# Kernel tuning notes

Measured on AMD Instinct MI355X. Metric: run time of the kernel, lower is better.

The kernel has to match this reference:

```python
import jax, jax.numpy as jnp
import numpy as np

N = 40000      # nodes
E = 640000     # edges
IN_C = 128
HID = 256
OUT_C = 10
G = 64         # graphs in batch


def setup_inputs() -> dict:
    key = jax.random.key(0)
    ks = jax.random.split(key, 8)
    x = jax.random.normal(ks[0], (N, IN_C), dtype=jnp.float32)
    edge_index = jax.random.randint(ks[1], (2, E), 0, N, dtype=jnp.int64)
    batch = jnp.sort(jax.random.randint(ks[2], (N,), 0, G, dtype=jnp.int64))
    W1 = jax.random.normal(ks[3], (IN_C, HID), dtype=jnp.float32) / np.sqrt(IN_C)
    b1 = jnp.zeros((HID,), dtype=jnp.float32)
    W2 = jax.random.normal(ks[4], (HID, HID), dtype=jnp.float32) / np.sqrt(HID)
    b2 = jnp.zeros((HID,), dtype=jnp.float32)
    Wlin = jax.random.normal(ks[5], (HID, OUT_C), dtype=jnp.float32) / np.sqrt(HID)
    blin = jnp.zeros((OUT_C,), dtype=jnp.float32)
    return {"x": x, "edge_index": edge_index, "batch": batch,
            "W1": W1, "b1": b1, "W2": W2, "b2": b2, "Wlin": Wlin, "blin": blin}


def _gcn_conv(x, W, b, src, dst, n_nodes):
    # PyG GCNConv: linear transform, self-loop-augmented sym normalization, scatter-add, bias
    h = x @ W                                   # [N, F]
    deg = jnp.zeros((n_nodes,), h.dtype).at[dst].add(1.0)  # in-degree incl. self loops
    dis = jax.lax.rsqrt(jnp.maximum(deg, 1.0))             # deg >= 1 due to self loops
    norm = dis[src] * dis[dst]                  # [E+N]
    msg = h[src] * norm[:, None]                # gather + scale
    out = jnp.zeros((n_nodes, h.shape[1]), h.dtype).at[dst].add(msg)
    return out + b


def reference(x, edge_index, batch, W1, b1, W2, b2, Wlin, blin):
    n = x.shape[0]
    loop = jnp.arange(n, dtype=edge_index.dtype)
    src = jnp.concatenate([edge_index[0], loop])  # add self loops (PyG default)
    dst = jnp.concatenate([edge_index[1], loop])

    h = jax.nn.relu(_gcn_conv(x, W1, b1, src, dst, n))
    h = jax.nn.relu(_gcn_conv(h, W2, b2, src, dst, n))

    # global_mean_pool over graph ids
    sums = jax.ops.segment_sum(h, batch, num_segments=G)            # [G, HID]
    cnts = jax.ops.segment_sum(jnp.ones((n,), h.dtype), batch, num_segments=G)
    pooled = sums / jnp.maximum(cnts, 1.0)[:, None]

    return pooled @ Wlin + blin                  # [G, OUT_C]
```

## Files before the change

kernel.cpp:

```cpp
#include <hip/hip_runtime.h>

#define NN    40000
#define EE    640000
#define INC   128
#define HID   256
#define OUTC  10
#define GG    64
#define CAP   64

typedef unsigned short u16;
typedef __attribute__((ext_vector_type(8))) short short8;
typedef __attribute__((ext_vector_type(4))) float f32x4;

__device__ __forceinline__ float bf2f(u16 h) {
    return __uint_as_float(((unsigned)h) << 16);
}
__device__ __forceinline__ u16 f2bf(float f) {
    unsigned u = __float_as_uint(f);
    unsigned r = u + 0x7FFFu + ((u >> 16) & 1u);
    return (u16)(r >> 16);
}

__device__ __forceinline__ void gload_lds16(const u16* g, u16* l) {
    __builtin_amdgcn_global_load_lds(
        (const __attribute__((address_space(1))) unsigned int*)g,
        (__attribute__((address_space(3))) unsigned int*)l,
        16, 0, 0);
}

#define WTOT (INC * HID + HID * HID)
__global__ void build_kernel(const int* __restrict__ src, const int* __restrict__ dst,
                             int* __restrict__ cnt, u16* __restrict__ col, int e4,
                             const float* __restrict__ W1, u16* __restrict__ w1h,
                             u16* __restrict__ w1l,
                             const float* __restrict__ W2, u16* __restrict__ w2h,
                             u16* __restrict__ w2l) {
    int i = blockIdx.x * blockDim.x + threadIdx.x;
    if (i < e4) {
        int4 d = ((const int4*)dst)[i];
        int4 s = ((const int4*)src)[i];
        int r0 = atomicAdd(&cnt[d.x], 1);
        int r1 = atomicAdd(&cnt[d.y], 1);
        int r2 = atomicAdd(&cnt[d.z], 1);
        int r3 = atomicAdd(&cnt[d.w], 1);
        if (r0 < CAP) col[(d.x << 6) + r0] = (u16)s.x;
        if (r1 < CAP) col[(d.y << 6) + r1] = (u16)s.y;
        if (r2 < CAP) col[(d.z << 6) + r2] = (u16)s.z;
        if (r3 < CAP) col[(d.w << 6) + r3] = (u16)s.w;
    } else if (i < e4 + WTOT) {
        int idx = i - e4;
        const float* W; u16 *Th, *Tl; int K;
        if (idx < INC * HID) { W = W1; Th = w1h; Tl = w1l; K = INC; }
        else { W = W2; Th = w2h; Tl = w2l; K = HID; idx -= INC * HID; }
        int k = idx >> 8;
        int n = idx & 255;
        float w = W[idx];
        u16 h = f2bf(w);
        float r = w - bf2f(h);
        Th[(size_t)n * K + k] = h;
        Tl[(size_t)n * K + k] = f2bf(r);
    }
}

__global__ __launch_bounds__(256) void xscale_kernel(
    const float* __restrict__ x, const int* __restrict__ cnt,
    u16* __restrict__ xs, int total4) {
    int j = blockIdx.x * blockDim.x + threadIdx.x;
    if (j >= total4) return;
    int n = j >> 5;
    float dn = rsqrtf((float)(cnt[n] + 1));
    float4 v = ((const float4*)x)[j];
    ushort4 o;
    o.x = f2bf(v.x * dn); o.y = f2bf(v.y * dn);
    o.z = f2bf(v.z * dn); o.w = f2bf(v.w * dn);
    ((ushort4*)xs)[j] = o;
}

#define BM 128
#define BN 128
#define BK 32
#define PGL 8

template<int MODE>
__global__ __launch_bounds__(256) void mgemm_kernel(
    const u16* __restrict__ A,
    const u16* __restrict__ Bh,
    const u16* __restrict__ Bl,
    const float* __restrict__ bias,
    const int* __restrict__ cnt,
    u16* __restrict__ Cout,
    const int* __restrict__ batch, float* __restrict__ pooled,
    int M, int K)
{
    __shared__ __align__(16) u16 As [BM * BK];
    __shared__ __align__(16) u16 Bhs[BN * BK];
    __shared__ __align__(16) u16 Bls[BN * BK];
    __shared__ float ptile[MODE == 1 ? PGL * BN : 1];

    const int tid  = threadIdx.x;
    const int lane = tid & 63;
    const int wave = tid >> 6;
    const int ln   = lane & 15;
    const int qd   = lane >> 4;
    const int wm   = (wave & 1) * 64;
    const int wn   = (wave >> 1) * 64;
    const int m0   = blockIdx.x * BM;
    const int n0   = blockIdx.y * BN;

    f32x4 acc[4][4];
#pragma unroll
    for (int i = 0; i < 4; ++i)
#pragma unroll
        for (int j = 0; j < 4; ++j) acc[i][j] = (f32x4)(0.0f);

    if (MODE == 1) {
        for (int t = tid; t < PGL * BN; t += 256) ptile[t] = 0.0f;
    }

    const int rl = lane >> 2;
    const int su = lane & 3;
    const int fsw = (qd ^ (ln & 3) ^ ((ln >> 2) & 3)) * 8;

    for (int k0 = 0; k0 < K; k0 += BK) {
#pragma unroll
        for (int L = 0; L < 2; ++L) {
            int rloc = (wave * 2 + L) * 16 + rl;
            int sw   = (su ^ (rloc & 3) ^ ((rloc >> 2) & 3)) * 8;
            int ga   = m0 + rloc; if (ga >= M) ga = M - 1;
            gload_lds16(A  + (size_t)ga * K        + k0 + sw, As  + (size_t)(wave * 2 + L) * 512);
            gload_lds16(Bh + (size_t)(n0 + rloc) * K + k0 + sw, Bhs + (size_t)(wave * 2 + L) * 512);
            gload_lds16(Bl + (size_t)(n0 + rloc) * K + k0 + sw, Bls + (size_t)(wave * 2 + L) * 512);
        }
        __syncthreads();

        short8 af[4], bfh[4], bfl[4];
#pragma unroll
        for (int t = 0; t < 4; ++t) {
            af[t]  = *(const short8*)(As  + (wm + t * 16 + ln) * BK + fsw);
            bfh[t] = *(const short8*)(Bhs + (wn + t * 16 + ln) * BK + fsw);
            bfl[t] = *(const short8*)(Bls + (wn + t * 16 + ln) * BK + fsw);
        }
#pragma unroll
        for (int ti = 0; ti < 4; ++ti)
#pragma unroll
            for (int tj = 0; tj < 4; ++tj) {
                acc[ti][tj] = __builtin_amdgcn_mfma_f32_16x16x32_bf16(
                    af[ti], bfh[tj], acc[ti][tj], 0, 0, 0);
                acc[ti][tj] = __builtin_amdgcn_mfma_f32_16x16x32_bf16(
                    af[ti], bfl[tj], acc[ti][tj], 0, 0, 0);
            }
        __syncthreads();
    }

    float bcol[4];
#pragma unroll
    for (int tj = 0; tj < 4; ++tj) bcol[tj] = bias[n0 + wn + tj * 16 + ln];

    if (MODE == 0) {
#pragma unroll
        for (int ti = 0; ti < 4; ++ti) {
#pragma unroll
            for (int r = 0; r < 4; ++r) {
                int row = m0 + wm + ti * 16 + qd * 4 + r;
                if (row < M) {
                    float dm = rsqrtf((float)(cnt[row] + 1));
                    u16* crow = Cout + (size_t)row * HID;
#pragma unroll
                    for (int tj = 0; tj < 4; ++tj) {
                        float v = fmaxf(acc[ti][tj][r] + bcol[tj], 0.0f);
                        crow[n0 + wn + tj * 16 + ln] = f2bf(v * dm);
                    }
                }
            }
        }
    } else {
        int bg[16];
#pragma unroll
        for (int ti = 0; ti < 4; ++ti)
#pragma unroll
            for (int r = 0; r < 4; ++r) {
                int row = m0 + wm + ti * 16 + qd * 4 + r;
                bg[ti * 4 + r] = (row < M) ? batch[row] : -1;
            }
        const int g_lo = batch[m0];
        const int g_hi = batch[min(m0 + BM, M) - 1];
        for (int g = g_lo; g <= g_hi; ++g) {
            float cs[4] = {0.0f, 0.0f, 0.0f, 0.0f};
#pragma unroll
            for (int ti = 0; ti < 4; ++ti)
#pragma unroll
                for (int r = 0; r < 4; ++r)
                    if (bg[ti * 4 + r] == g) {
#pragma unroll
                        for (int tj = 0; tj < 4; ++tj)
                            cs[tj] += fmaxf(acc[ti][tj][r] + bcol[tj], 0.0f);
                    }
#pragma unroll
            for (int tj = 0; tj < 4; ++tj) {
                cs[tj] += __shfl_xor(cs[tj], 16);
                cs[tj] += __shfl_xor(cs[tj], 32);
            }
            if (qd == 0) {
                int gl = g - g_lo;
#pragma unroll
                for (int tj = 0; tj < 4; ++tj) {
                    int c = wn + tj * 16 + ln;
                    if (gl < PGL) atomicAdd(&ptile[gl * BN + c], cs[tj]);
                    else atomicAdd(&pooled[(size_t)g * HID + n0 + c], cs[tj]);
                }
            }
        }
        __syncthreads();
        const int g0 = batch[m0];
        for (int t = tid; t < PGL * BN; t += 256) {
            float v = ptile[t];
            if (v != 0.0f) {
                int gl = t / BN, c = t % BN;
                atomicAdd(&pooled[(size_t)(g0 + gl) * HID + n0 + c], v);
            }
        }
    }
}

template<int F>
__global__ __launch_bounds__(256) void agg_kernel(
    const u16* __restrict__ hs, const int* __restrict__ cnt,
    const u16* __restrict__ col, u16* __restrict__ out, int n_nodes)
{
    constexpr int L  = F / 8;
    constexpr int G  = 64 / L;
    constexpr int UF = 16 / G;
    const int lane = threadIdx.x & 63;
    const int n    = (blockIdx.x * blockDim.x + threadIdx.x) >> 6;
    if (n >= n_nodes) return;
    const int li = lane % L;
    const int gi = lane / L;

    const int base0 = n << 6;
    const int total = 1 + cnt[n];

    float acc[8];
#pragma unroll
    for (int i = 0; i < 8; ++i) acc[i] = 0.0f;

    for (int base = 0; base < total; base += G * UF) {
        int  idxs[UF];
        bool valid[UF];
#pragma unroll
        for (int u = 0; u < UF; ++u) {
            int it = base + u * G + gi;
            valid[u] = (it < total);
            idxs[u] = 0;
            if (valid[u]) idxs[u] = (it == 0) ? n : (int)col[base0 + it - 1];
        }
        uint4 w[UF];
#pragma unroll
        for (int u = 0; u < UF; ++u)
            if (valid[u])
                w[u] = *(const uint4*)(hs + (size_t)idxs[u] * F + li * 8);
#pragma unroll
        for (int u = 0; u < UF; ++u)
            if (valid[u]) {
                unsigned uu[4] = {w[u].x, w[u].y, w[u].z, w[u].w};
#pragma unroll
                for (int q = 0; q < 4; ++q) {
                    acc[2 * q]     += __uint_as_float(uu[q] << 16);
                    acc[2 * q + 1] += __uint_as_float(uu[q] & 0xFFFF0000u);
                }
            }
    }

#pragma unroll
    for (int off = 32; off >= L; off >>= 1)
#pragma unroll
        for (int i = 0; i < 8; ++i)
            acc[i] += __shfl_xor(acc[i], off);

    if (gi == 0) {
        float d = rsqrtf((float)total);
        unsigned r[4];
#pragma unroll
        for (int q = 0; q < 4; ++q) {
            unsigned l16 = (unsigned)f2bf(acc[2 * q] * d);
            unsigned h16 = (unsigned)f2bf(acc[2 * q + 1] * d);
            r[q] = l16 | (h16 << 16);
        }
        *(uint4*)(out + (size_t)n * F + li * 8) = make_uint4(r[0], r[1], r[2], r[3]);
    }
}

__global__ __launch_bounds__(256) void pool_finalize_kernel(
    const float* __restrict__ pooled, const int* __restrict__ batch,
    const float* __restrict__ Wlin, const float* __restrict__ blin,
    float* __restrict__ out, int n_nodes)
{
    const int g = blockIdx.x;
    const int j = threadIdx.x;
    int lo = 0, hi = n_nodes;
    while (lo < hi) { int mid = (lo + hi) >> 1; if (batch[mid] < g) lo = mid + 1; else hi = mid; }
    const int start = lo;
    lo = start; hi = n_nodes;
    while (lo < hi) { int mid = (lo + hi) >> 1; if (batch[mid] < g + 1) lo = mid + 1; else hi = mid; }
    const int cnt = lo - start;

    float pv = pooled[(size_t)g * HID + j] / fmaxf((float)cnt, 1.0f);

    __shared__ float pl[HID];
    pl[j] = pv;
    __syncthreads();
    if (j < OUTC) {
        float o = blin[j];
        for (int k = 0; k < HID; ++k) o = fmaf(pl[k], Wlin[k * OUTC + j], o);
        out[g * OUTC + j] = o;
    }
}

extern "C" void kernel_launch(void* const* d_in, const int* in_sizes, int n_in,
                              void* d_out, int out_size, void* d_ws, size_t ws_size,
                              hipStream_t stream) {
    const float* x     = (const float*)d_in[0];
    const int*   ei    = (const int*)  d_in[1];
    const int*   batch = (const int*)  d_in[2];
    const float* W1    = (const float*)d_in[3];
    const float* b1    = (const float*)d_in[4];
    const float* W2    = (const float*)d_in[5];
    const float* b2    = (const float*)d_in[6];
    const float* Wlin  = (const float*)d_in[7];
    const float* blin  = (const float*)d_in[8];
    float* out = (float*)d_out;

    const int* src = ei;
    const int* dst = ei + EE;

    char* p = (char*)d_ws;
    u16*   xs  = (u16*)p;   p += (size_t)NN * INC * sizeof(u16);
    u16*   xab = (u16*)p;   p += (size_t)NN * INC * sizeof(u16);
    u16*   h1s = (u16*)p;   p += (size_t)NN * HID * sizeof(u16);
    u16*   a2b = (u16*)p;   p += (size_t)NN * HID * sizeof(u16);
    u16*   w1h = (u16*)p;   p += (size_t)HID * INC * sizeof(u16);
    u16*   w1l = (u16*)p;   p += (size_t)HID * INC * sizeof(u16);
    u16*   w2h = (u16*)p;   p += (size_t)HID * HID * sizeof(u16);
    u16*   w2l = (u16*)p;   p += (size_t)HID * HID * sizeof(u16);
    char* zbase = p;
    float* pooled = (float*)p; p += (size_t)GG * HID * sizeof(float);
    int* cnt    = (int*)p;  p += (size_t)NN * sizeof(int);
    size_t zbytes = (size_t)(p - zbase);
    u16* col    = (u16*)p;  p += (size_t)NN * CAP * sizeof(u16);
    (void)ws_size; (void)n_in; (void)in_sizes; (void)out_size;

    const int TB = 256;
    const int e4     = EE / 4;
    const int total4 = NN * INC / 4;
    const int build_threads = e4 + WTOT;
    const int nb_build = (build_threads + TB - 1) / TB;

    hipMemsetAsync(zbase, 0, zbytes, stream);
    build_kernel<<<nb_build, TB, 0, stream>>>(src, dst, cnt, col, e4,
                                              W1, w1h, w1l, W2, w2h, w2l);
    xscale_kernel<<<(total4 + TB - 1) / TB, TB, 0, stream>>>(x, cnt, xs, total4);

    dim3 ggrid((NN + BM - 1) / BM, HID / BN);
    const int agg_blocks = (NN * 64 + TB - 1) / TB;

    agg_kernel<INC><<<agg_blocks, TB, 0, stream>>>(xs, cnt, col, xab, NN);
    mgemm_kernel<0><<<ggrid, 256, 0, stream>>>(xab, w1h, w1l, b1, cnt, h1s,
                                               batch, pooled, NN, INC);

    agg_kernel<HID><<<agg_blocks, TB, 0, stream>>>(h1s, cnt, col, a2b, NN);
    mgemm_kernel<1><<<ggrid, 256, 0, stream>>>(a2b, w2h, w2l, b2, cnt, (u16*)nullptr,
                                               batch, pooled, NN, HID);

    pool_finalize_kernel<<<GG, 256, 0, stream>>>(pooled, batch, Wlin, blin, out, NN);
}
```

Baseline: 241.8 us.

## Restructure aggregation into per-wave 4-node feature-slice tiles

The aggregation kernel now gives each wave four nodes and a 32-column feature slice. Sixteen lane groups walk the neighbour lists in parallel, and each lane issues four independent 16-byte gathers per iteration. Blocks are interleaved across slices via the blockIdx low bits so that feature slices of neighbouring node chunks share cache locality. The aim is more memory-level parallelism and better L2 reuse of gathered rows. In exchange it does wasted work when the four nodes have unequal degrees, and it assumes NN is divisible by 16 and the slice mapping fits 8 virtual blocks.

```diff
diff --git a/kernel.cpp b/kernel.cpp
--- a/kernel.cpp
+++ b/kernel.cpp
@@ -227,65 +227,75 @@
     const u16* __restrict__ hs, const int* __restrict__ cnt,
     const u16* __restrict__ col, u16* __restrict__ out, int n_nodes)
 {
-    constexpr int L  = F / 8;
-    constexpr int G  = 64 / L;
-    constexpr int UF = 16 / G;
-    const int lane = threadIdx.x & 63;
-    const int n    = (blockIdx.x * blockDim.x + threadIdx.x) >> 6;
-    if (n >= n_nodes) return;
-    const int li = lane % L;
-    const int gi = lane / L;
-
-    const int base0 = n << 6;
-    const int total = 1 + cnt[n];
-
-    float acc[8];
-#pragma unroll
-    for (int i = 0; i < 8; ++i) acc[i] = 0.0f;
-
-    for (int base = 0; base < total; base += G * UF) {
-        int  idxs[UF];
-        bool valid[UF];
-#pragma unroll
-        for (int u = 0; u < UF; ++u) {
-            int it = base + u * G + gi;
-            valid[u] = (it < total);
-            idxs[u] = 0;
-            if (valid[u]) idxs[u] = (it == 0) ? n : (int)col[base0 + it - 1];
-        }
-        uint4 w[UF];
-#pragma unroll
-        for (int u = 0; u < UF; ++u)
-            if (valid[u])
-                w[u] = *(const uint4*)(hs + (size_t)idxs[u] * F + li * 8);
-#pragma unroll
-        for (int u = 0; u < UF; ++u)
-            if (valid[u]) {
-                unsigned uu[4] = {w[u].x, w[u].y, w[u].z, w[u].w};
+    constexpr int NSL = F / 32;
+    const int tid  = threadIdx.x;
+    const int lane = tid & 63;
+    const int wave = tid >> 6;
+    const int gi   = lane >> 2;
+    const int li   = lane & 3;
+    const int virt  = blockIdx.x & 7;
+    const int slice = virt % NSL;
+    const int nchunk = (blockIdx.x >> 3) * (8 / NSL) + virt / NSL;
+    const int nb = nchunk * 16 + wave * 4;
+
+    int cn[4];
+#pragma unroll
+    for (int u = 0; u < 4; ++u) cn[u] = cnt[nb + u];
+    const int tmax = max(max(cn[0], cn[1]), max(cn[2], cn[3])) + 1;
+
+    float acc[4][8];
+#pragma unroll
+    for (int u = 0; u < 4; ++u)
+#pragma unroll
+        for (int i = 0; i < 8; ++i) acc[u][i] = 0.0f;
+
+    const u16* hsl = hs + slice * 32 + li * 8;
+
+    for (int base = 0; base < tmax; base += 16) {
+        const int it = base + gi;
+        int idx[4]; bool val[4];
+#pragma unroll
+        for (int u = 0; u < 4; ++u) {
+            val[u] = (it <= cn[u]);
+            int ci = ((nb + u) << 6) + min(max(it - 1, 0), 63);
+            int v  = (it == 0) ? (nb + u) : (int)col[ci];
+            idx[u] = val[u] ? v : (nb + u);
+        }
+        uint4 g[4];
+#pragma unroll
+        for (int u = 0; u < 4; ++u)
+            g[u] = *(const uint4*)(hsl + (size_t)idx[u] * F);
+#pragma unroll
+        for (int u = 0; u < 4; ++u)
+            if (val[u]) {
+                unsigned uu[4] = {g[u].x, g[u].y, g[u].z, g[u].w};
 #pragma unroll
                 for (int q = 0; q < 4; ++q) {
-                    acc[2 * q]     += __uint_as_float(uu[q] << 16);
-                    acc[2 * q + 1] += __uint_as_float(uu[q] & 0xFFFF0000u);
+                    acc[u][2 * q]     += __uint_as_float(uu[q] << 16);
+                    acc[u][2 * q + 1] += __uint_as_float(uu[q] & 0xFFFF0000u);
                 }
             }
     }
 
 #pragma unroll
-    for (int off = 32; off >= L; off >>= 1)
-#pragma unroll
-        for (int i = 0; i < 8; ++i)
-            acc[i] += __shfl_xor(acc[i], off);
+    for (int u = 0; u < 4; ++u)
+#pragma unroll
+        for (int off = 4; off <= 32; off <<= 1)
+#pragma unroll
+            for (int i = 0; i < 8; ++i)
+                acc[u][i] += __shfl_xor(acc[u][i], off);
 
     if (gi == 0) {
-        float d = rsqrtf((float)total);
-        unsigned r[4];
-#pragma unroll
-        for (int q = 0; q < 4; ++q) {
-            unsigned l16 = (unsigned)f2bf(acc[2 * q] * d);
-            unsigned h16 = (unsigned)f2bf(acc[2 * q + 1] * d);
-            r[q] = l16 | (h16 << 16);
-        }
-        *(uint4*)(out + (size_t)n * F + li * 8) = make_uint4(r[0], r[1], r[2], r[3]);
+#pragma unroll
+        for (int u = 0; u < 4; ++u) {
+            float dn = rsqrtf((float)(cn[u] + 1));
+            uint4 r;
+            r.x = (unsigned)f2bf(acc[u][0] * dn) | ((unsigned)f2bf(acc[u][1] * dn) << 16);
+            r.y = (unsigned)f2bf(acc[u][2] * dn) | ((unsigned)f2bf(acc[u][3] * dn) << 16);
+            r.z = (unsigned)f2bf(acc[u][4] * dn) | ((unsigned)f2bf(acc[u][5] * dn) << 16);
+            r.w = (unsigned)f2bf(acc[u][6] * dn) | ((unsigned)f2bf(acc[u][7] * dn) << 16);
+            *(uint4*)(out + (size_t)(nb + u) * F + slice * 32 + li * 8) = r;
+        }
     }
 }
 
@@ -360,13 +370,14 @@
     xscale_kernel<<<(total4 + TB - 1) / TB, TB, 0, stream>>>(x, cnt, xs, total4);
 
     dim3 ggrid((NN + BM - 1) / BM, HID / BN);
-    const int agg_blocks = (NN * 64 + TB - 1) / TB;
-
-    agg_kernel<INC><<<agg_blocks, TB, 0, stream>>>(xs, cnt, col, xab, NN);
+    const int agg1_blocks = (NN / 16) * (INC / 32);
+    const int agg2_blocks = (NN / 16) * (HID / 32);
+
+    agg_kernel<INC><<<agg1_blocks, TB, 0, stream>>>(xs, cnt, col, xab, NN);
     mgemm_kernel<0><<<ggrid, 256, 0, stream>>>(xab, w1h, w1l, b1, cnt, h1s,
                                                batch, pooled, NN, INC);
 
-    agg_kernel<HID><<<agg_blocks, TB, 0, stream>>>(h1s, cnt, col, a2b, NN);
+    agg_kernel<HID><<<agg2_blocks, TB, 0, stream>>>(h1s, cnt, col, a2b, NN);
     mgemm_kernel<1><<<ggrid, 256, 0, stream>>>(a2b, w2h, w2l, b2, cnt, (u16*)nullptr,
                                                batch, pooled, NN, HID);
 
```

Measured after the change: 337.8 us. 1.4x slower.

## Slice layer-2 aggregation by feature columns with XCC-affine persistent work queues

Applied to the files above, without the earlier changes.

Replaces the second-layer neighbor aggregation with a persistent kernel that splits the 256-wide features into four 64-column slices. Each slice has its own atomic work counter, and blocks prefer the slice matching their XCC id. The goal is for each XCC's L2 to hold a smaller slice of the gathered feature table, so random gathers hit cache more often. The cost is atomic work-stealing overhead, narrower 8-byte gathers, and a 16-node serial loop per wave, which may reduce memory-level parallelism.

```diff
diff --git a/kernel.cpp b/kernel.cpp
--- a/kernel.cpp
+++ b/kernel.cpp
@@ -289,6 +289,84 @@
     }
 }
 
+#define SL_CH    64
+#define SL_NSL   4
+#define SL_UNITS (NN / SL_CH)
+__global__ __launch_bounds__(256) void agg2_sliced_kernel(
+    const u16* __restrict__ hs, const int* __restrict__ cnt,
+    const u16* __restrict__ col, u16* __restrict__ out,
+    int* __restrict__ ctr)
+{
+    __shared__ int s_unit;
+    const int tid  = threadIdx.x;
+    const int lane = tid & 63;
+    const int wave = tid >> 6;
+    const int gi   = lane >> 4;
+    const int li   = lane & 15;
+    const int xcc  = __builtin_amdgcn_s_getreg((31 << 11) | 20) & 7;
+    const int pref = xcc & (SL_NSL - 1);
+
+    for (;;) {
+        if (tid == 0) {
+            int u = -1;
+            for (int s = 0; s < SL_NSL && u < 0; ++s) {
+                int sl = (pref + s) & (SL_NSL - 1);
+                int c  = atomicAdd(&ctr[sl], 1);
+                if (c < SL_UNITS) u = sl * SL_UNITS + c;
+            }
+            s_unit = u;
+        }
+        __syncthreads();
+        const int unit = s_unit;
+        if (unit < 0) break;
+        const int slice = unit / SL_UNITS;
+        const int chunk = unit - slice * SL_UNITS;
+        const u16* hsl = hs + slice * 64 + li * 4;
+        const int nb = chunk * SL_CH + wave * 16;
+
+        for (int u2 = 0; u2 < 16; ++u2) {
+            const int node = nb + u2;
+            const int cn   = cnt[node];
+            const int cb   = node << 6;
+            float a0 = 0.0f, a1 = 0.0f, a2 = 0.0f, a3 = 0.0f;
+            for (int b = 0; b <= cn; b += 8) {
+                int it0 = b + gi, it1 = b + 4 + gi;
+                bool v0 = (it0 <= cn), v1 = (it1 <= cn);
+                int i0 = node, i1 = node;
+                if (v0 && it0 > 0) i0 = (int)col[cb + it0 - 1];
+                if (v1)            i1 = (int)col[cb + it1 - 1];
+                if (!v1)           i1 = node;
+                uint2 g0 = *(const uint2*)(hsl + (size_t)i0 * HID);
+                uint2 g1 = *(const uint2*)(hsl + (size_t)i1 * HID);
+                if (v0) {
+                    a0 += __uint_as_float(g0.x << 16);
+                    a1 += __uint_as_float(g0.x & 0xFFFF0000u);
+                    a2 += __uint_as_float(g0.y << 16);
+                    a3 += __uint_as_float(g0.y & 0xFFFF0000u);
+                }
+                if (v1) {
+                    a0 += __uint_as_float(g1.x << 16);
+                    a1 += __uint_as_float(g1.x & 0xFFFF0000u);
+                    a2 += __uint_as_float(g1.y << 16);
+                    a3 += __uint_as_float(g1.y & 0xFFFF0000u);
+                }
+            }
+            a0 += __shfl_xor(a0, 16); a0 += __shfl_xor(a0, 32);
+            a1 += __shfl_xor(a1, 16); a1 += __shfl_xor(a1, 32);
+            a2 += __shfl_xor(a2, 16); a2 += __shfl_xor(a2, 32);
+            a3 += __shfl_xor(a3, 16); a3 += __shfl_xor(a3, 32);
+            if (gi == 0) {
+                float dn = rsqrtf((float)(cn + 1));
+                uint2 r;
+                r.x = (unsigned)f2bf(a0 * dn) | ((unsigned)f2bf(a1 * dn) << 16);
+                r.y = (unsigned)f2bf(a2 * dn) | ((unsigned)f2bf(a3 * dn) << 16);
+                *(uint2*)(out + (size_t)node * HID + slice * 64 + li * 4) = r;
+            }
+        }
+        __syncthreads();
+    }
+}
+
 __global__ __launch_bounds__(256) void pool_finalize_kernel(
     const float* __restrict__ pooled, const int* __restrict__ batch,
     const float* __restrict__ Wlin, const float* __restrict__ blin,
@@ -343,6 +421,7 @@
     u16*   w2l = (u16*)p;   p += (size_t)HID * HID * sizeof(u16);
     char* zbase = p;
     float* pooled = (float*)p; p += (size_t)GG * HID * sizeof(float);
+    int* ctr    = (int*)p;  p += SL_NSL * sizeof(int);
     int* cnt    = (int*)p;  p += (size_t)NN * sizeof(int);
     size_t zbytes = (size_t)(p - zbase);
     u16* col    = (u16*)p;  p += (size_t)NN * CAP * sizeof(u16);
@@ -366,7 +445,7 @@
     mgemm_kernel<0><<<ggrid, 256, 0, stream>>>(xab, w1h, w1l, b1, cnt, h1s,
                                                batch, pooled, NN, INC);
 
-    agg_kernel<HID><<<agg_blocks, TB, 0, stream>>>(h1s, cnt, col, a2b, NN);
+    agg2_sliced_kernel<<<2048, TB, 0, stream>>>(h1s, cnt, col, a2b, ctr);
     mgemm_kernel<1><<<ggrid, 256, 0, stream>>>(a2b, w2h, w2l, b2, cnt, (u16*)nullptr,
                                                batch, pooled, NN, HID);
 
```

Measured after the change: 378.5 us. 56.5% more time.
